# Kernel tuning notes

Measured on AMD Instinct MI355X. Metric: run time of the kernel, lower is better.

## Reference

```python
import jax, jax.numpy as jnp
import numpy as np

B, N, D = 4, 1024, 1024      # batch, seq_len, query_dim
H, DH = 16, 64               # heads, dim_head; inner = H*DH = 1024
INNER = H * DH
SCALE = DH ** -0.5


def setup_inputs() -> dict:
    key = jax.random.key(0)
    ks = jax.random.split(key, 8)
    x = jax.random.normal(ks[0], (B, N, D), dtype=jnp.float32)
    rel_pos = jax.random.normal(ks[1], (B * H, N, N), dtype=jnp.float32)
    query_mask = jax.random.randint(ks[2], (B, N), 0, 2).astype(bool)
    context_mask = jax.random.randint(ks[3], (B, N), 0, 2).astype(bool)
    # Linear weights stored (in, out); to_q/to_kv have no bias, to_out has bias.
    Wq = jax.random.normal(ks[4], (D, INNER), dtype=jnp.float32) / np.sqrt(D)
    Wkv = jax.random.normal(ks[5], (D, 2 * INNER), dtype=jnp.float32) / np.sqrt(D)
    Wo = jax.random.normal(ks[6], (INNER, D), dtype=jnp.float32) / np.sqrt(INNER)
    bo = jax.random.normal(ks[7], (D,), dtype=jnp.float32) * 0.01
    return {"x": x, "rel_pos": rel_pos, "query_mask": query_mask,
            "context_mask": context_mask, "Wq": Wq, "Wkv": Wkv, "Wo": Wo, "bo": bo}


def reference(x, rel_pos, query_mask, context_mask, Wq, Wkv, Wo, bo):
    # Self-attention (context = x)
    q = x @ Wq                                 # [B, N, INNER]
    kv = x @ Wkv                               # [B, N, 2*INNER]
    k, v = jnp.split(kv, 2, axis=-1)
    # (b n (h d)) -> (b h n d)
    split_heads = lambda t: t.reshape(B, N, H, DH).transpose(0, 2, 1, 3)
    q, k, v = map(split_heads, (q, k, v))
    sim = jnp.einsum('bhid,bhjd->bhij', q, k) * SCALE
    sim = sim + rel_pos.reshape(B, H, N, N)
    neg = -jnp.finfo(sim.dtype).max
    # query_mask: (b i) -> mask rows; context_mask: (b j) -> mask cols
    sim = jnp.where(query_mask[:, None, :, None], sim, neg)
    sim = jnp.where(context_mask[:, None, None, :], sim, neg)
    attn = jax.nn.softmax(sim, axis=-1)
    out = jnp.einsum('bhij,bhjd->bhid', attn, v)    # [B, H, N, DH]
    out = out.transpose(0, 2, 1, 3).reshape(B, N, INNER)
    return out @ Wo + bo
```

## Files before the change

### kernel.cpp

```cpp
#include <hip/hip_runtime.h>


#define NEGMAX 3.402823466e+38f

typedef short short8 __attribute__((ext_vector_type(8)));
typedef float f32x4 __attribute__((ext_vector_type(4)));

__device__ __forceinline__ unsigned short f2bf(float f) {
  unsigned int u = __float_as_uint(f);
  u += 0x7FFFu + ((u >> 16) & 1u);
  return (unsigned short)(u >> 16);
}

__device__ __forceinline__ void stage16(const void* g, void* lds_base, int lane) {
#if __has_builtin(__builtin_amdgcn_global_load_lds)
  __builtin_amdgcn_global_load_lds(
      (const __attribute__((address_space(1))) unsigned int*)g,
      (__attribute__((address_space(3))) unsigned int*)lds_base, 16, 0, 0);
#else
  *(int4*)((char*)lds_base + lane * 16) = *(const int4*)g;
#endif
}

__global__ void cast_x_k(const float* __restrict__ x, unsigned short* __restrict__ xb) {
  int i = (blockIdx.x * 256 + threadIdx.x) * 4;
  float4 v = *(const float4*)(x + i);
  ushort4 o;
  o.x = f2bf(v.x); o.y = f2bf(v.y); o.z = f2bf(v.z); o.w = f2bf(v.w);
  *(ushort4*)(xb + i) = o;
}

__global__ __launch_bounds__(256) void tcast_k(const float* __restrict__ src, int ldsrc,
                                               unsigned short* __restrict__ dst) {
  __shared__ float T[64][65];
  const int n0 = blockIdx.x * 64, d0 = blockIdx.y * 64;
  const int tx = threadIdx.x & 63, ty = threadIdx.x >> 6;
#pragma unroll
  for (int k = 0; k < 16; ++k) {
    int dl = k * 4 + ty;
    T[dl][tx] = src[(size_t)(d0 + dl) * ldsrc + n0 + tx];
  }
  __syncthreads();
#pragma unroll
  for (int k = 0; k < 16; ++k) {
    int nl = k * 4 + ty;
    dst[(size_t)(n0 + nl) * 1024 + d0 + tx] = f2bf(T[tx][nl]);
  }
}

template <int MODE>
__global__ __launch_bounds__(256) void gemm_bt_k(
    const unsigned short* __restrict__ A, const unsigned short* __restrict__ Bt,
    unsigned short* __restrict__ qws, unsigned short* __restrict__ kws,
    unsigned short* __restrict__ vtws,
    const float* __restrict__ bias, float* __restrict__ Cout) {
  constexpr int K = 1024;
  constexpr int NKB = K / 32;
  __shared__ alignas(16) unsigned short As[128 * 32];
  __shared__ alignas(16) unsigned short Bs[128 * 32];
  const int tid = threadIdx.x;
  const int lane = tid & 63, w = tid >> 6;
  const int quad = lane >> 4, lanelo = lane & 15;
  const int tRow = blockIdx.y * 128, tCol = blockIdx.x * 128;
  const int wr = (w >> 1) * 64, wc = (w & 1) * 64;
  const char* AgB = (const char*)(A + (size_t)tRow * K);
  const char* BgB = (const char*)(Bt + (size_t)tCol * K);
  const int c0 = tid, c1 = tid + 256;
  const size_t a0off = (size_t)(c0 >> 2) * 2048 + (c0 & 3) * 16;
  const size_t a1off = (size_t)(c1 >> 2) * 2048 + (c1 & 3) * 16;
  char* ldsA0 = (char*)As + w * 1024;
  char* ldsA1 = (char*)As + 4096 + w * 1024;
  char* ldsB0 = (char*)Bs + w * 1024;
  char* ldsB1 = (char*)Bs + 4096 + w * 1024;

  f32x4 acc[4][4];
#pragma unroll
  for (int i = 0; i < 4; ++i)
#pragma unroll
    for (int j = 0; j < 4; ++j) acc[i][j] = (f32x4){0.f, 0.f, 0.f, 0.f};

  for (int kb = 0; kb < NKB; ++kb) {
    if (kb) __syncthreads();
    const size_t ko = (size_t)kb * 64;
    stage16(AgB + a0off + ko, ldsA0, lane);
    stage16(AgB + a1off + ko, ldsA1, lane);
    stage16(BgB + a0off + ko, ldsB0, lane);
    stage16(BgB + a1off + ko, ldsB1, lane);
    __syncthreads();

    short8 af[4], bf[4];
#pragma unroll
    for (int i = 0; i < 4; ++i)
      af[i] = *(const short8*)(As + (wr + i * 16 + lanelo) * 32 + quad * 8);
#pragma unroll
    for (int j = 0; j < 4; ++j)
      bf[j] = *(const short8*)(Bs + (wc + j * 16 + lanelo) * 32 + quad * 8);
#pragma unroll
    for (int i = 0; i < 4; ++i)
#pragma unroll
      for (int j = 0; j < 4; ++j)
        acc[i][j] = __builtin_amdgcn_mfma_f32_16x16x32_bf16(af[i], bf[j], acc[i][j], 0, 0, 0);
  }

  if (MODE == 0) {
#pragma unroll
    for (int i = 0; i < 4; ++i) {
      int row = tRow + wr + i * 16 + quad * 4;
      int b_ = row >> 10;
      int npos = row & 1023;
#pragma unroll
      for (int j = 0; j < 4; ++j) {
        int col = tCol + wc + j * 16 + lanelo;
        if (col < 2048) {
          unsigned short* dst = (col < 1024) ? qws : kws;
          int c = col & 1023;
          int hh = c >> 6, dh = c & 63;
          size_t base = ((size_t)(b_ * 16 + hh) * 1024 + npos) * 64 + dh;
#pragma unroll
          for (int r = 0; r < 4; ++r) dst[base + (size_t)r * 64] = f2bf(acc[i][j][r]);
        } else {
          int c = col - 2048;
          ushort4 pk;
          pk.x = f2bf(acc[i][j][0]);
          pk.y = f2bf(acc[i][j][1]);
          pk.z = f2bf(acc[i][j][2]);
          pk.w = f2bf(acc[i][j][3]);
          *(ushort4*)&vtws[((size_t)(b_ * 16 + (c >> 6)) * 64 + (c & 63)) * 1024 + npos] = pk;
        }
      }
    }
  } else {
#pragma unroll
    for (int i = 0; i < 4; ++i) {
      int row = tRow + wr + i * 16 + quad * 4;
#pragma unroll
      for (int j = 0; j < 4; ++j) {
        int col = tCol + wc + j * 16 + lanelo;
        float bv = bias[col];
#pragma unroll
        for (int r = 0; r < 4; ++r)
          Cout[(size_t)(row + r) * 1024 + col] = acc[i][j][r] + bv;
      }
    }
  }
}

__global__ __launch_bounds__(256) void attn_k(
    const unsigned short* __restrict__ q_ws, const unsigned short* __restrict__ k_ws,
    const unsigned short* __restrict__ vt_ws, const float* __restrict__ rel,
    const int* __restrict__ qmask, const int* __restrict__ cmask,
    unsigned short* __restrict__ aout) {
  constexpr float SCALE = 0.125f;
  __shared__ alignas(16) unsigned short Kl[64 * 72];
  __shared__ alignas(16) unsigned short Vl[64 * 72];
  __shared__ alignas(16) unsigned short Pl[4 * 16 * 72];
  __shared__ float cml[1024];

  const int tid = threadIdx.x;
  const int w = tid >> 6, lane = tid & 63;
  const int quad = lane >> 4, lanelo = lane & 15;
  const int bh = blockIdx.y, b_ = bh >> 4, h = bh & 15;
  const int qrow0 = blockIdx.x * 64 + w * 16;

  for (int i = tid; i < 1024; i += 256)
    cml[i] = (cmask[b_ * 1024 + i] != 0) ? 1.f : 0.f;

  const unsigned short* qg = q_ws + ((size_t)bh * 1024 + qrow0) * 64;
  short8 qf0 = *(const short8*)(qg + (size_t)lanelo * 64 + quad * 8);
  short8 qf1 = *(const short8*)(qg + (size_t)lanelo * 64 + 32 + quad * 8);

  float qmv[4];
#pragma unroll
  for (int r = 0; r < 4; ++r)
    qmv[r] = (qmask[b_ * 1024 + qrow0 + quad * 4 + r] != 0) ? 1.f : 0.f;

  f32x4 o[4];
#pragma unroll
  for (int g = 0; g < 4; ++g) o[g] = (f32x4){0.f, 0.f, 0.f, 0.f};
  float m_run[4], l_run[4];
#pragma unroll
  for (int r = 0; r < 4; ++r) { m_run[r] = -NEGMAX; l_run[r] = 0.f; }

  const char* kgB = (const char*)(k_ws + (size_t)bh * 65536);
  const char* vgB = (const char*)(vt_ws + (size_t)bh * 65536);
  const float* relg = rel + ((size_t)bh * 1024 + qrow0) * 1024;
  unsigned short* pw = Pl + w * 16 * 72;

  const int k0 = tid >> 3, ch0 = tid & 7;
  int4 kc0 = *(const int4*)(kgB + (size_t)k0 * 128 + ch0 * 16);
  int4 kc1 = *(const int4*)(kgB + (size_t)(k0 + 32) * 128 + ch0 * 16);
  int4 vc0 = *(const int4*)(vgB + (size_t)k0 * 2048 + ch0 * 16);
  int4 vc1 = *(const int4*)(vgB + (size_t)(k0 + 32) * 2048 + ch0 * 16);

  float rl[4][4];
#pragma unroll
  for (int r = 0; r < 4; ++r)
#pragma unroll
    for (int c = 0; c < 4; ++c)
      rl[r][c] = relg[(size_t)(quad * 4 + r) * 1024 + c * 16 + lanelo];

  for (int kb = 0; kb < 16; ++kb) {
    __syncthreads();
    *(int4*)((char*)Kl + k0 * 144 + ch0 * 16) = kc0;
    *(int4*)((char*)Kl + (k0 + 32) * 144 + ch0 * 16) = kc1;
    *(int4*)((char*)Vl + k0 * 144 + ch0 * 16) = vc0;
    *(int4*)((char*)Vl + (k0 + 32) * 144 + ch0 * 16) = vc1;
    __syncthreads();
    if (kb + 1 < 16) {
      const size_t kof = (size_t)(kb + 1) * 64;
      kc0 = *(const int4*)(kgB + (kof + k0) * 128 + ch0 * 16);
      kc1 = *(const int4*)(kgB + (kof + k0 + 32) * 128 + ch0 * 16);
      vc0 = *(const int4*)(vgB + (size_t)k0 * 2048 + kof * 2 + ch0 * 16);
      vc1 = *(const int4*)(vgB + (size_t)(k0 + 32) * 2048 + kof * 2 + ch0 * 16);
    }

    f32x4 s[4];
#pragma unroll
    for (int c = 0; c < 4; ++c) {
      s[c] = (f32x4){0.f, 0.f, 0.f, 0.f};
      short8 kfa = *(const short8*)((const char*)Kl + (c * 16 + lanelo) * 144 + quad * 16);
      s[c] = __builtin_amdgcn_mfma_f32_16x16x32_bf16(qf0, kfa, s[c], 0, 0, 0);
      short8 kfb = *(const short8*)((const char*)Kl + (c * 16 + lanelo) * 144 + 64 + quad * 16);
      s[c] = __builtin_amdgcn_mfma_f32_16x16x32_bf16(qf1, kfb, s[c], 0, 0, 0);
    }

    float rln[4][4];
    if (kb + 1 < 16) {
#pragma unroll
      for (int r = 0; r < 4; ++r)
#pragma unroll
        for (int c = 0; c < 4; ++c)
          rln[r][c] = relg[(size_t)(quad * 4 + r) * 1024 + (kb + 1) * 64 + c * 16 + lanelo];
    }

    float cm[4];
#pragma unroll
    for (int c = 0; c < 4; ++c) cm[c] = cml[kb * 64 + c * 16 + lanelo];

#pragma unroll
    for (int r = 0; r < 4; ++r) {
      const bool qok = qmv[r] != 0.f;
      float x[4], mloc = -NEGMAX;
#pragma unroll
      for (int c = 0; c < 4; ++c) {
        x[c] = (qok && cm[c] != 0.f) ? s[c][r] * SCALE + rl[r][c] : -NEGMAX;
        mloc = fmaxf(mloc, x[c]);
      }
      for (int off = 1; off < 16; off <<= 1) mloc = fmaxf(mloc, __shfl_xor(mloc, off));
      float mnew = fmaxf(m_run[r], mloc);
      float alpha = __expf(m_run[r] - mnew);
      m_run[r] = mnew;
      float ps = 0.f;
      unsigned short pb[4];
#pragma unroll
      for (int c = 0; c < 4; ++c) {
        float p = __expf(x[c] - mnew);
        ps += p;
        pb[c] = f2bf(p);
      }
      for (int off = 1; off < 16; off <<= 1) ps += __shfl_xor(ps, off);
      l_run[r] = l_run[r] * alpha + ps;
#pragma unroll
      for (int g = 0; g < 4; ++g) o[g][r] *= alpha;
#pragma unroll
      for (int c = 0; c < 4; ++c) pw[(quad * 4 + r) * 72 + c * 16 + lanelo] = pb[c];
    }

    if (kb + 1 < 16) {
#pragma unroll
      for (int r = 0; r < 4; ++r)
#pragma unroll
        for (int c = 0; c < 4; ++c) rl[r][c] = rln[r][c];
    }

#pragma unroll
    for (int c2 = 0; c2 < 2; ++c2) {
      short8 pa = *(const short8*)((const char*)pw + lanelo * 144 + c2 * 64 + quad * 16);
#pragma unroll
      for (int g = 0; g < 4; ++g) {
        short8 vb = *(const short8*)((const char*)Vl + (g * 16 + lanelo) * 144 + c2 * 64 + quad * 16);
        o[g] = __builtin_amdgcn_mfma_f32_16x16x32_bf16(pa, vb, o[g], 0, 0, 0);
      }
    }
  }

#pragma unroll
  for (int r = 0; r < 4; ++r) {
    float inv = 1.f / l_run[r];
    size_t row = (size_t)(b_ * 1024 + qrow0 + quad * 4 + r) * 1024;
#pragma unroll
    for (int g = 0; g < 4; ++g)
      aout[row + h * 64 + g * 16 + lanelo] = f2bf(o[g][r] * inv);
  }
}

extern "C" void kernel_launch(void* const* d_in, const int* in_sizes, int n_in,
                              void* d_out, int out_size, void* d_ws, size_t ws_size,
                              hipStream_t stream) {
  const float* x = (const float*)d_in[0];
  const float* rel = (const float*)d_in[1];
  const int* qmask = (const int*)d_in[2];
  const int* cmask = (const int*)d_in[3];
  const float* Wq = (const float*)d_in[4];
  const float* Wkv = (const float*)d_in[5];
  const float* Wo = (const float*)d_in[6];
  const float* bo = (const float*)d_in[7];
  float* out = (float*)d_out;

  char* ws = (char*)d_ws;
  const size_t MB = 1024 * 1024;
  unsigned short* w3t = (unsigned short*)(ws);
  unsigned short* wot = (unsigned short*)(ws + 6 * MB);
  unsigned short* xb  = (unsigned short*)(ws + 8 * MB);
  unsigned short* qws = (unsigned short*)(ws + 16 * MB);
  unsigned short* kws = (unsigned short*)(ws + 24 * MB);
  unsigned short* vtws = (unsigned short*)(ws + 32 * MB);
  unsigned short* aout = xb;

  cast_x_k<<<4096, 256, 0, stream>>>(x, xb);
  tcast_k<<<dim3(16, 16), 256, 0, stream>>>(Wq, 1024, w3t);
  tcast_k<<<dim3(32, 16), 256, 0, stream>>>(Wkv, 2048, w3t + (size_t)1024 * 1024);
  tcast_k<<<dim3(16, 16), 256, 0, stream>>>(Wo, 1024, wot);
  gemm_bt_k<0><<<dim3(24, 32), 256, 0, stream>>>(xb, w3t, qws, kws, vtws, nullptr, nullptr);
  attn_k<<<dim3(16, 64), 256, 0, stream>>>(qws, kws, vtws, rel, qmask, cmask, aout);
  gemm_bt_k<1><<<dim3(8, 32), 256, 0, stream>>>(aout, wot, nullptr, nullptr, nullptr, bo, out);
}
```

Before: 489.1 us.

## Read K/V fragments directly from global memory and remap blocks for L2 locality

Removes the LDS staging of K and V tiles, the per-iteration block barriers and the register prefetch. Each wave now loads its MFMA fragments straight from global memory. The block index is remapped so that consecutive blocks on the same XCD share a head and its K/V stay cached, and the launch bounds request higher occupancy. In exchange, each wave issues redundant global loads and loses the software prefetch of rel_pos and K/V, relying on caches and occupancy to hide latency.

```diff
diff --git a/kernel.cpp b/kernel.cpp
--- a/kernel.cpp
+++ b/kernel.cpp
@@ -145,25 +145,28 @@
   }
 }
 
-__global__ __launch_bounds__(256) void attn_k(
+__global__ __launch_bounds__(256, 4) void attn_k(
     const unsigned short* __restrict__ q_ws, const unsigned short* __restrict__ k_ws,
     const unsigned short* __restrict__ vt_ws, const float* __restrict__ rel,
     const int* __restrict__ qmask, const int* __restrict__ cmask,
     unsigned short* __restrict__ aout) {
   constexpr float SCALE = 0.125f;
-  __shared__ alignas(16) unsigned short Kl[64 * 72];
-  __shared__ alignas(16) unsigned short Vl[64 * 72];
   __shared__ alignas(16) unsigned short Pl[4 * 16 * 72];
   __shared__ float cml[1024];
 
   const int tid = threadIdx.x;
   const int w = tid >> 6, lane = tid & 63;
   const int quad = lane >> 4, lanelo = lane & 15;
-  const int bh = blockIdx.y, b_ = bh >> 4, h = bh & 15;
-  const int qrow0 = blockIdx.x * 64 + w * 16;
+
+  const int flat = blockIdx.y * 16 + blockIdx.x;
+  const int virt = (flat & 7) * 128 + (flat >> 3);
+  const int bh = virt >> 4, qblk = virt & 15;
+  const int b_ = bh >> 4, h = bh & 15;
+  const int qrow0 = qblk * 64 + w * 16;
 
   for (int i = tid; i < 1024; i += 256)
     cml[i] = (cmask[b_ * 1024 + i] != 0) ? 1.f : 0.f;
+  __syncthreads();
 
   const unsigned short* qg = q_ws + ((size_t)bh * 1024 + qrow0) * 64;
   short8 qf0 = *(const short8*)(qg + (size_t)lanelo * 64 + quad * 8);
@@ -181,61 +184,34 @@
 #pragma unroll
   for (int r = 0; r < 4; ++r) { m_run[r] = -NEGMAX; l_run[r] = 0.f; }
 
-  const char* kgB = (const char*)(k_ws + (size_t)bh * 65536);
-  const char* vgB = (const char*)(vt_ws + (size_t)bh * 65536);
+  const unsigned short* kg = k_ws + (size_t)bh * 65536;
+  const unsigned short* vg = vt_ws + (size_t)bh * 65536;
   const float* relg = rel + ((size_t)bh * 1024 + qrow0) * 1024;
   unsigned short* pw = Pl + w * 16 * 72;
 
-  const int k0 = tid >> 3, ch0 = tid & 7;
-  int4 kc0 = *(const int4*)(kgB + (size_t)k0 * 128 + ch0 * 16);
-  int4 kc1 = *(const int4*)(kgB + (size_t)(k0 + 32) * 128 + ch0 * 16);
-  int4 vc0 = *(const int4*)(vgB + (size_t)k0 * 2048 + ch0 * 16);
-  int4 vc1 = *(const int4*)(vgB + (size_t)(k0 + 32) * 2048 + ch0 * 16);
-
-  float rl[4][4];
-#pragma unroll
-  for (int r = 0; r < 4; ++r)
-#pragma unroll
-    for (int c = 0; c < 4; ++c)
-      rl[r][c] = relg[(size_t)(quad * 4 + r) * 1024 + c * 16 + lanelo];
-
   for (int kb = 0; kb < 16; ++kb) {
-    __syncthreads();
-    *(int4*)((char*)Kl + k0 * 144 + ch0 * 16) = kc0;
-    *(int4*)((char*)Kl + (k0 + 32) * 144 + ch0 * 16) = kc1;
-    *(int4*)((char*)Vl + k0 * 144 + ch0 * 16) = vc0;
-    *(int4*)((char*)Vl + (k0 + 32) * 144 + ch0 * 16) = vc1;
-    __syncthreads();
-    if (kb + 1 < 16) {
-      const size_t kof = (size_t)(kb + 1) * 64;
-      kc0 = *(const int4*)(kgB + (kof + k0) * 128 + ch0 * 16);
-      kc1 = *(const int4*)(kgB + (kof + k0 + 32) * 128 + ch0 * 16);
-      vc0 = *(const int4*)(vgB + (size_t)k0 * 2048 + kof * 2 + ch0 * 16);
-      vc1 = *(const int4*)(vgB + (size_t)(k0 + 32) * 2048 + kof * 2 + ch0 * 16);
-    }
+    const int key0 = kb * 64;
 
     f32x4 s[4];
 #pragma unroll
     for (int c = 0; c < 4; ++c) {
+      const unsigned short* krow = kg + (size_t)(key0 + c * 16 + lanelo) * 64;
+      short8 kfa = *(const short8*)(krow + quad * 8);
+      short8 kfb = *(const short8*)(krow + 32 + quad * 8);
       s[c] = (f32x4){0.f, 0.f, 0.f, 0.f};
-      short8 kfa = *(const short8*)((const char*)Kl + (c * 16 + lanelo) * 144 + quad * 16);
       s[c] = __builtin_amdgcn_mfma_f32_16x16x32_bf16(qf0, kfa, s[c], 0, 0, 0);
-      short8 kfb = *(const short8*)((const char*)Kl + (c * 16 + lanelo) * 144 + 64 + quad * 16);
       s[c] = __builtin_amdgcn_mfma_f32_16x16x32_bf16(qf1, kfb, s[c], 0, 0, 0);
     }
 
-    float rln[4][4];
-    if (kb + 1 < 16) {
-#pragma unroll
-      for (int r = 0; r < 4; ++r)
-#pragma unroll
-        for (int c = 0; c < 4; ++c)
-          rln[r][c] = relg[(size_t)(quad * 4 + r) * 1024 + (kb + 1) * 64 + c * 16 + lanelo];
-    }
-
+    float rl[4][4];
+#pragma unroll
+    for (int r = 0; r < 4; ++r)
+#pragma unroll
+      for (int c = 0; c < 4; ++c)
+        rl[r][c] = relg[(size_t)(quad * 4 + r) * 1024 + key0 + c * 16 + lanelo];
     float cm[4];
 #pragma unroll
-    for (int c = 0; c < 4; ++c) cm[c] = cml[kb * 64 + c * 16 + lanelo];
+    for (int c = 0; c < 4; ++c) cm[c] = cml[key0 + c * 16 + lanelo];
 
 #pragma unroll
     for (int r = 0; r < 4; ++r) {
@@ -266,19 +242,12 @@
       for (int c = 0; c < 4; ++c) pw[(quad * 4 + r) * 72 + c * 16 + lanelo] = pb[c];
     }
 
-    if (kb + 1 < 16) {
-#pragma unroll
-      for (int r = 0; r < 4; ++r)
-#pragma unroll
-        for (int c = 0; c < 4; ++c) rl[r][c] = rln[r][c];
-    }
-
 #pragma unroll
     for (int c2 = 0; c2 < 2; ++c2) {
       short8 pa = *(const short8*)((const char*)pw + lanelo * 144 + c2 * 64 + quad * 16);
 #pragma unroll
       for (int g = 0; g < 4; ++g) {
-        short8 vb = *(const short8*)((const char*)Vl + (g * 16 + lanelo) * 144 + c2 * 64 + quad * 16);
+        short8 vb = *(const short8*)(vg + (size_t)(g * 16 + lanelo) * 1024 + key0 + c2 * 32 + quad * 8);
         o[g] = __builtin_amdgcn_mfma_f32_16x16x32_bf16(pa, vb, o[g], 0, 0, 0);
       }
     }
```

New measurement: 550.1 us. 12.5% more time.
